# Kernel optimization log

Hardware: AMD Instinct MI355X
Metric: run time of the kernel (lower is better)

## Reference

```python
import jax, jax.numpy as jnp
import numpy as np

N = 50000      # nodes
E = 800000     # edges (avg degree 16)
HID = 64       # hidden / out_channels per head (concat=False)
EDIM = 3       # edge_dim
H = 4          # heads
C = 64         # per-head channels (== hidden since concat=False mean)
L = 2          # ode_layers
NEG_SLOPE = 0.2
LN_EPS = 1e-5


def setup_inputs() -> dict:
    key = jax.random.key(0)
    ks = jax.random.split(key, 12)
    h = jax.random.normal(ks[0], (N, HID), dtype=jnp.float32)
    edge_index = jax.random.randint(ks[1], (2, E), 0, N, dtype=jnp.int64)
    edge_attr = jax.random.normal(ks[2], (E, EDIM), dtype=jnp.float32)
    t = jnp.zeros((), dtype=jnp.float32)
    s = 1.0 / np.sqrt(HID)
    lin_W = jax.random.normal(ks[3], (L, H * C, HID), dtype=jnp.float32) * s
    lin_W = lin_W.at[L - 1].mul(0.1)  # mimics gats[-1].lin.weight.mul_(0.1)
    lin_edge_W = jax.random.normal(ks[4], (L, H * C, EDIM), dtype=jnp.float32) * (1.0 / np.sqrt(EDIM))
    att_src = jax.random.normal(ks[5], (L, H, C), dtype=jnp.float32) * s
    att_dst = jax.random.normal(ks[6], (L, H, C), dtype=jnp.float32) * s
    att_edge = jax.random.normal(ks[7], (L, H, C), dtype=jnp.float32) * s
    bias = jnp.zeros((L, C), dtype=jnp.float32)
    ln_gamma = jnp.ones((L, HID), dtype=jnp.float32)
    ln_beta = jnp.zeros((L, HID), dtype=jnp.float32)
    return {"t": t, "h": h, "edge_index": edge_index, "edge_attr": edge_attr,
            "lin_W": lin_W, "lin_edge_W": lin_edge_W, "att_src": att_src,
            "att_dst": att_dst, "att_edge": att_edge, "bias": bias,
            "ln_gamma": ln_gamma, "ln_beta": ln_beta}


def _gat_layer(z, src, dst, lin_W, lin_edge_W, att_src, att_dst, att_edge,
               bias, edge_attr):
    n = z.shape[0]
    x = (z @ lin_W.T).reshape(n, H, C)                      # [N,H,C]
    a_src = (x * att_src).sum(-1)                            # [N,H]
    a_dst = (x * att_dst).sum(-1)                            # [N,H]
    e = (edge_attr @ lin_edge_W.T).reshape(-1, H, C)         # [E,H,C]
    a_e = (e * att_edge).sum(-1)                             # [E,H]
    alpha = jax.nn.leaky_relu(a_src[src] + a_dst[dst] + a_e, NEG_SLOPE)
    # segment-softmax over incoming edges of each destination node
    amax = jax.ops.segment_max(alpha, dst, num_segments=n)
    amax = jnp.where(jnp.isfinite(amax), amax, 0.0)
    ex = jnp.exp(alpha - amax[dst])                          # [E,H]
    denom = jax.ops.segment_sum(ex, dst, num_segments=n)
    w = ex / (denom[dst] + 1e-16)
    msg = jax.ops.segment_sum(w[:, :, None] * x[src], dst, num_segments=n)
    return msg.mean(axis=1) + bias                           # [N,C] (concat=False)


def reference(t, h, edge_index, edge_attr, lin_W, lin_edge_W, att_src,
              att_dst, att_edge, bias, ln_gamma, ln_beta):
    src, dst = edge_index[0], edge_index[1]
    z = h
    for i in range(L):
        out = _gat_layer(z, src, dst, lin_W[i], lin_edge_W[i], att_src[i],
                         att_dst[i], att_edge[i], bias[i], edge_attr)
        mu = out.mean(-1, keepdims=True)
        var = ((out - mu) ** 2).mean(-1, keepdims=True)
        ln = (out - mu) / jnp.sqrt(var + LN_EPS) * ln_gamma[i] + ln_beta[i]
        z = jax.nn.silu(ln)
    return z
```

## Files before the change

### kernel.cpp

```cpp
#include <hip/hip_runtime.h>
#include <math.h>

#define NN 50000
#define NE 800000
#define NEG_SLOPE 0.2f
#define LN_EPS 1e-5f
#define SROW 264

typedef unsigned short ushort_t;
typedef unsigned int uint_t;
typedef __attribute__((ext_vector_type(8))) short bf16x8;
typedef __attribute__((ext_vector_type(4))) float f32x4;

__device__ __forceinline__ float bf2f(ushort_t u) {
    return __uint_as_float(((uint_t)u) << 16);
}
__device__ __forceinline__ ushort_t f2bf(float f) {
    uint_t b = __float_as_uint(f);
    uint_t r = (b + 0x7fffu + ((b >> 16) & 1u)) >> 16;
    return (ushort_t)r;
}
__device__ __forceinline__ float ldx(const void* p, size_t i, int isbf) {
    return isbf ? bf2f(((const ushort_t*)p)[i]) : ((const float*)p)[i];
}
__device__ __forceinline__ int clampN(int v) {
    return v < 0 ? 0 : (v >= NN ? NN - 1 : v);
}
__device__ __forceinline__ int sniff_f64(const int* ei) {
    return (ei[1] == 0 && ei[3] == 0 && ei[5] == 0 && ei[7] == 0) ? 1 : 0;
}

__global__ __launch_bounds__(256) void setup(
    const void* __restrict__ lin_W, const void* __restrict__ lin_edge_W,
    const void* __restrict__ att_src, const void* __restrict__ att_dst,
    const void* __restrict__ att_edge, const void* __restrict__ h_in,
    const int* __restrict__ ei, float* __restrict__ Mbuf,
    ushort_t* __restrict__ wext, int* __restrict__ esrc, int* __restrict__ edst,
    int* __restrict__ deg, int* __restrict__ pos, int* __restrict__ flags) {
    int tid = threadIdx.x, lane = tid & 63;
    int nthreads = gridDim.x * 256;
    int gtid = blockIdx.x * 256 + tid;
    __shared__ int s_bf;
    if (tid == 0) s_bf = 1;
    __syncthreads();
    {
        uint_t ex = (((const ushort_t*)h_in)[2 * tid] >> 7) & 0xFFu;
        if (ex > 0x8Cu) s_bf = 0;
    }
    __syncthreads();
    int isbf = s_bf;
    int f64 = sniff_f64(ei);
    if (gtid == 0) {
        flags[0] = f64;
        flags[1] = isbf;
    }
    if (f64) {
        const int4* s4 = (const int4*)ei;
        const int4* d4 = (const int4*)(ei + 2 * NE);
        for (int p = gtid; p < NE / 2; p += nthreads) {
            int4 sv = s4[p], dv = d4[p];
            int d0 = clampN(dv.x), d1 = clampN(dv.z);
            esrc[2 * p]     = clampN(sv.x);
            esrc[2 * p + 1] = clampN(sv.z);
            edst[2 * p]     = d0;
            edst[2 * p + 1] = d1;
            pos[2 * p]      = atomicAdd(&deg[d0], 1);
            pos[2 * p + 1]  = atomicAdd(&deg[d1], 1);
        }
    } else {
        const int2* s2 = (const int2*)ei;
        const int2* d2 = (const int2*)(ei + NE);
        for (int p = gtid; p < NE / 2; p += nthreads) {
            int2 sv = s2[p], dv = d2[p];
            int d0 = clampN(dv.x), d1 = clampN(dv.y);
            esrc[2 * p]     = clampN(sv.x);
            esrc[2 * p + 1] = clampN(sv.y);
            edst[2 * p]     = d0;
            edst[2 * p + 1] = d1;
            pos[2 * p]      = atomicAdd(&deg[d0], 1);
            pos[2 * p + 1]  = atomicAdd(&deg[d1], 1);
        }
    }
    if (blockIdx.x == 0) {
        for (int rep = 0; rep < 2; ++rep) {
            int idx = rep * 256 + tid;
            int l = idx >> 8, hc = idx & 255;
            float ae = ldx(att_edge, l * 256 + hc, isbf);
            size_t b3 = ((size_t)l * 256 + hc) * 3;
            float q0 = ae * ldx(lin_edge_W, b3 + 0, isbf);
            float q1 = ae * ldx(lin_edge_W, b3 + 1, isbf);
            float q2 = ae * ldx(lin_edge_W, b3 + 2, isbf);
            for (int off = 32; off > 0; off >>= 1) {
                q0 += __shfl_down(q0, off);
                q1 += __shfl_down(q1, off);
                q2 += __shfl_down(q2, off);
            }
            if (lane == 0) {
                int h = (idx >> 6) & 3;
                Mbuf[(l * 4 + h) * 3 + 0] = q0;
                Mbuf[(l * 4 + h) * 3 + 1] = q1;
                Mbuf[(l * 4 + h) * 3 + 2] = q2;
            }
        }
    }
    for (int idx = gtid; idx < 2 * 272 * 64; idx += nthreads) {
        int d = idx & 63;
        int row = (idx >> 6) % 272;
        int l = idx / (272 * 64);
        float v = 0.f;
        if (row < 256) {
            v = ldx(lin_W, ((size_t)l * 256 + row) * 64 + d, isbf);
        } else if (row < 264) {
            int h = (row - 256) & 3;
            const void* att = (row < 260) ? att_src : att_dst;
            float v0 = 0.f, v1 = 0.f, v2 = 0.f, v3 = 0.f;
            for (int c = 0; c < 64; c += 4) {
                size_t wb = ((size_t)l * 256 + h * 64 + c) * 64 + d;
                size_t ab = (size_t)l * 256 + h * 64 + c;
                v0 += ldx(lin_W, wb,       isbf) * ldx(att, ab,     isbf);
                v1 += ldx(lin_W, wb + 64,  isbf) * ldx(att, ab + 1, isbf);
                v2 += ldx(lin_W, wb + 128, isbf) * ldx(att, ab + 2, isbf);
                v3 += ldx(lin_W, wb + 192, isbf) * ldx(att, ab + 3, isbf);
            }
            v = (v0 + v1) + (v2 + v3);
        }
        wext[((size_t)l * 272 + row) * 64 + d] = f2bf(v);
    }
}


template <int LAYER>
__device__ __forceinline__ void linear_body(
    int bid, int nblk, const void* __restrict__ h_in,
    const ushort_t* __restrict__ zbuf, const ushort_t* __restrict__ wext,
    ushort_t* __restrict__ xb, float* __restrict__ a_src,
    float* __restrict__ a_dst, int isbf) {
    __shared__ __align__(16) ushort_t st_all[4 * 16 * SROW];
    int tid = threadIdx.x, wv = tid >> 6, lane = tid & 63;
    int q = lane >> 4, mi = lane & 15;
    int f32path = (LAYER == 0) && !isbf;
    const ushort_t* zsrc = (LAYER == 0) ? (const ushort_t*)h_in : zbuf;
    const ushort_t* wl = wext + (size_t)LAYER * 272 * 64;
    bf16x8 wf[34];
#pragma unroll
    for (int t = 0; t < 17; ++t) {
        const ushort_t* wrow = wl + (size_t)(t * 16 + mi) * 64;
        wf[2 * t]     = *(const bf16x8*)(wrow + q * 8);
        wf[2 * t + 1] = *(const bf16x8*)(wrow + 32 + q * 8);
    }
    ushort_t* st = st_all + wv * 16 * SROW;
    int gwave = bid * 4 + wv, nwaves = nblk * 4;
    for (int tile = gwave; tile < NN / 16; tile += nwaves) {
        int mbase = tile * 16, mynode = mbase + mi;
        bf16x8 b0, b1;
        if (f32path) {
            const float* zf = (const float*)h_in + (size_t)mynode * 64;
            float4 fa = *(const float4*)(zf + q * 8);
            float4 fb = *(const float4*)(zf + q * 8 + 4);
            float4 fc = *(const float4*)(zf + 32 + q * 8);
            float4 fd = *(const float4*)(zf + 32 + q * 8 + 4);
            b0[0] = (short)f2bf(fa.x); b0[1] = (short)f2bf(fa.y);
            b0[2] = (short)f2bf(fa.z); b0[3] = (short)f2bf(fa.w);
            b0[4] = (short)f2bf(fb.x); b0[5] = (short)f2bf(fb.y);
            b0[6] = (short)f2bf(fb.z); b0[7] = (short)f2bf(fb.w);
            b1[0] = (short)f2bf(fc.x); b1[1] = (short)f2bf(fc.y);
            b1[2] = (short)f2bf(fc.z); b1[3] = (short)f2bf(fc.w);
            b1[4] = (short)f2bf(fd.x); b1[5] = (short)f2bf(fd.y);
            b1[6] = (short)f2bf(fd.z); b1[7] = (short)f2bf(fd.w);
        } else {
            const ushort_t* zrow = zsrc + (size_t)mynode * 64;
            b0 = *(const bf16x8*)(zrow + q * 8);
            b1 = *(const bf16x8*)(zrow + 32 + q * 8);
        }
#pragma unroll
        for (int t = 0; t < 17; ++t) {
            f32x4 acc = {0.f, 0.f, 0.f, 0.f};
            acc = __builtin_amdgcn_mfma_f32_16x16x32_bf16(wf[2 * t], b0, acc, 0, 0, 0);
            acc = __builtin_amdgcn_mfma_f32_16x16x32_bf16(wf[2 * t + 1], b1, acc, 0, 0, 0);
            if (t < 16) {
                ushort4 pk;
                pk.x = f2bf(acc[0]);
                pk.y = f2bf(acc[1]);
                pk.z = f2bf(acc[2]);
                pk.w = f2bf(acc[3]);
                *(ushort4*)(st + mi * SROW + t * 16 + q * 4) = pk;
            } else {
                float4 av;
                av.x = acc[0]; av.y = acc[1]; av.z = acc[2]; av.w = acc[3];
                if (q == 0) *(float4*)(a_src + (size_t)mynode * 4) = av;
                else if (q == 1) *(float4*)(a_dst + (size_t)mynode * 4) = av;
            }
        }
        for (int nn = 0; nn < 16; ++nn) {
            int node = mbase + nn;
            ushort4 pk;
            pk.x = st[nn * SROW + lane];
            pk.y = st[nn * SROW + 64 + lane];
            pk.z = st[nn * SROW + 128 + lane];
            pk.w = st[nn * SROW + 192 + lane];
            *(ushort4*)(xb + (size_t)node * 256 + lane * 4) = pk;
        }
    }
}

__global__ __launch_bounds__(256) void scan_linear0(
    const int* __restrict__ deg, int* __restrict__ rowptr,
    const void* __restrict__ h_in, const ushort_t* __restrict__ wext,
    ushort_t* __restrict__ xb, float* __restrict__ a_src,
    float* __restrict__ a_dst, const int* __restrict__ flags) {
    if (blockIdx.x == 0) {
        __shared__ int sh[256];
        int tid = threadIdx.x;
        const int PER = 200;
        int base = tid * PER;
        int s = 0;
        if (tid < 250) {
            for (int i = 0; i < PER; ++i) s += deg[base + i];
        }
        sh[tid] = s;
        __syncthreads();
        for (int off = 1; off < 256; off <<= 1) {
            int t = (tid >= off) ? sh[tid - off] : 0;
            __syncthreads();
            sh[tid] += t;
            __syncthreads();
        }
        int excl = sh[tid] - s;
        if (tid < 250) {
            int run = excl;
            for (int i = 0; i < PER; ++i) {
                rowptr[base + i] = run;
                run += deg[base + i];
            }
        }
        if (tid == 255) rowptr[NN] = NE;
    } else {
        linear_body<0>(blockIdx.x - 1, gridDim.x - 1, h_in, (const ushort_t*)0,
                       wext, xb, a_src, a_dst, flags[1]);
    }
}

__global__ __launch_bounds__(256) void node_linear1(
    const ushort_t* __restrict__ zbuf, const ushort_t* __restrict__ wext,
    ushort_t* __restrict__ xb, float* __restrict__ a_src,
    float* __restrict__ a_dst, const int* __restrict__ flags) {
    linear_body<1>(blockIdx.x, gridDim.x, (const void*)0, zbuf, wext, xb,
                   a_src, a_dst, flags[1]);
}

__global__ void csr_fill(const int* __restrict__ esrc, const int* __restrict__ edst,
                         const void* __restrict__ edge_attr,
                         const int* __restrict__ rowptr, const int* __restrict__ pos,
                         float4* __restrict__ edata, const int* __restrict__ flags) {
    int e4 = blockIdx.x * 256 + threadIdx.x;
    if (e4 >= NE / 4) return;
    int isbf = flags[1];
    int e = e4 * 4;
    int4 sv = *(const int4*)(esrc + e);
    int4 dv = *(const int4*)(edst + e);
    int4 pv = *(const int4*)(pos + e);
    float a[12];
    if (!isbf) {
        const float4* ea = (const float4*)((const float*)edge_attr + (size_t)e * 3);
        float4 f0 = ea[0], f1 = ea[1], f2 = ea[2];
        a[0] = f0.x; a[1] = f0.y; a[2]  = f0.z;
        a[3] = f0.w; a[4] = f1.x; a[5]  = f1.y;
        a[6] = f1.z; a[7] = f1.w; a[8]  = f2.x;
        a[9] = f2.y; a[10] = f2.z; a[11] = f2.w;
    } else {
#pragma unroll
        for (int i = 0; i < 12; ++i)
            a[i] = bf2f(((const ushort_t*)edge_attr)[(size_t)e * 3 + i]);
    }
    float4 ed0, ed1, ed2, ed3;
    ed0.x = a[0]; ed0.y = a[1];  ed0.z = a[2];  ed0.w = __int_as_float(sv.x);
    ed1.x = a[3]; ed1.y = a[4];  ed1.z = a[5];  ed1.w = __int_as_float(sv.y);
    ed2.x = a[6]; ed2.y = a[7];  ed2.z = a[8];  ed2.w = __int_as_float(sv.z);
    ed3.x = a[9]; ed3.y = a[10]; ed3.z = a[11]; ed3.w = __int_as_float(sv.w);
    edata[rowptr[dv.x] + pv.x] = ed0;
    edata[rowptr[dv.y] + pv.y] = ed1;
    edata[rowptr[dv.z] + pv.z] = ed2;
    edata[rowptr[dv.w] + pv.w] = ed3;
}

__global__ __launch_bounds__(256) void node_aggregate(
    const int* __restrict__ rowptr, const float4* __restrict__ edata,
    const float* __restrict__ a_src, const float* __restrict__ a_dst,
    const ushort_t* __restrict__ xb, const float* __restrict__ Mbuf,
    const void* __restrict__ bias, const void* __restrict__ gamma,
    const void* __restrict__ beta, ushort_t* __restrict__ zout,
    void* __restrict__ outp, const int* __restrict__ flags, int layer, int last) {
    __shared__ float4 wsh[4][64];
    __shared__ int ssh[4][64];
    int isbf = flags[1];
    int wv = threadIdx.x >> 6;
    int lane = threadIdx.x & 63;
    int n = blockIdx.x * 4 + wv;
    float M[12];
#pragma unroll
    for (int i = 0; i < 12; ++i) M[i] = Mbuf[layer * 12 + i];
    float4 ad = *(const float4*)(a_dst + (size_t)n * 4);
    int start = rowptr[n], end = rowptr[n + 1];
    float acc0 = 0.f, acc1 = 0.f, acc2 = 0.f, acc3 = 0.f;
    float den0 = 0.f, den1 = 0.f, den2 = 0.f, den3 = 0.f;
    for (int cb = start; cb < end; cb += 64) {
        int m = end - cb;
        if (m > 64) m = 64;
        if (lane < m) {
            float4 ed = edata[cb + lane];
            int s = __float_as_int(ed.w);
            float4 as4 = *(const float4*)(a_src + (size_t)s * 4);
            float t0 = as4.x + ad.x + ed.x * M[0] + ed.y * M[1] + ed.z * M[2];
            float t1 = as4.y + ad.y + ed.x * M[3] + ed.y * M[4] + ed.z * M[5];
            float t2 = as4.z + ad.z + ed.x * M[6] + ed.y * M[7] + ed.z * M[8];
            float t3 = as4.w + ad.w + ed.x * M[9] + ed.y * M[10] + ed.z * M[11];
            t0 = t0 > 0.f ? t0 : NEG_SLOPE * t0;
            t1 = t1 > 0.f ? t1 : NEG_SLOPE * t1;
            t2 = t2 > 0.f ? t2 : NEG_SLOPE * t2;
            t3 = t3 > 0.f ? t3 : NEG_SLOPE * t3;
            float4 ex;
            ex.x = __expf(fminf(t0, 80.f));
            ex.y = __expf(fminf(t1, 80.f));
            ex.z = __expf(fminf(t2, 80.f));
            ex.w = __expf(fminf(t3, 80.f));
            wsh[wv][lane] = ex;
            ssh[wv][lane] = s;
        }
        for (int j = 0; j < m; j += 4) {
            int j1 = j + 1 < m ? j + 1 : m - 1;
            int j2 = j + 2 < m ? j + 2 : m - 1;
            int j3 = j + 3 < m ? j + 3 : m - 1;
            int s0 = ssh[wv][j],  s1 = ssh[wv][j1];
            int s2 = ssh[wv][j2], s3 = ssh[wv][j3];
            float4 w0 = wsh[wv][j];
            float4 w1 = wsh[wv][j1];
            float4 w2 = wsh[wv][j2];
            float4 w3 = wsh[wv][j3];
            if (j + 1 >= m) w1 = make_float4(0.f, 0.f, 0.f, 0.f);
            if (j + 2 >= m) w2 = make_float4(0.f, 0.f, 0.f, 0.f);
            if (j + 3 >= m) w3 = make_float4(0.f, 0.f, 0.f, 0.f);
            ushort4 x0 = *(const ushort4*)(xb + (size_t)s0 * 256 + lane * 4);
            ushort4 x1 = *(const ushort4*)(xb + (size_t)s1 * 256 + lane * 4);
            ushort4 x2 = *(const ushort4*)(xb + (size_t)s2 * 256 + lane * 4);
            ushort4 x3 = *(const ushort4*)(xb + (size_t)s3 * 256 + lane * 4);
            acc0 += w0.x * bf2f(x0.x) + w1.x * bf2f(x1.x) +
                    w2.x * bf2f(x2.x) + w3.x * bf2f(x3.x);
            acc1 += w0.y * bf2f(x0.y) + w1.y * bf2f(x1.y) +
                    w2.y * bf2f(x2.y) + w3.y * bf2f(x3.y);
            acc2 += w0.z * bf2f(x0.z) + w1.z * bf2f(x1.z) +
                    w2.z * bf2f(x2.z) + w3.z * bf2f(x3.z);
            acc3 += w0.w * bf2f(x0.w) + w1.w * bf2f(x1.w) +
                    w2.w * bf2f(x2.w) + w3.w * bf2f(x3.w);
            den0 += w0.x + w1.x + w2.x + w3.x;
            den1 += w0.y + w1.y + w2.y + w3.y;
            den2 += w0.z + w1.z + w2.z + w3.z;
            den3 += w0.w + w1.w + w2.w + w3.w;
        }
    }
    float v = ldx(bias, layer * 64 + lane, isbf) +
              0.25f * (acc0 / (den0 + 1e-16f) + acc1 / (den1 + 1e-16f) +
                       acc2 / (den2 + 1e-16f) + acc3 / (den3 + 1e-16f));
    float sum = v;
    for (int off = 1; off < 64; off <<= 1) sum += __shfl_xor(sum, off);
    float mu = sum * (1.f / 64.f);
    float d = v - mu;
    float vv = d * d;
    for (int off = 1; off < 64; off <<= 1) vv += __shfl_xor(vv, off);
    float var = vv * (1.f / 64.f);
    float ln = d * rsqrtf(var + LN_EPS) * ldx(gamma, layer * 64 + lane, isbf) +
               ldx(beta, layer * 64 + lane, isbf);
    float sl = ln / (1.f + __expf(-ln));
    size_t idx = (size_t)n * 64 + lane;
    if (last) {
        if (isbf) ((ushort_t*)outp)[idx] = f2bf(sl);
        else      ((float*)outp)[idx] = sl;
    } else {
        zout[idx] = f2bf(sl);
    }
}

extern "C" void kernel_launch(void* const* d_in, const int* in_sizes, int n_in,
                              void* d_out, int out_size, void* d_ws, size_t ws_size,
                              hipStream_t stream) {
    int off = (in_sizes[0] == 1) ? 1 : 0;
    const void* h_in  = d_in[off + 0];
    const int*  ei    = (const int*)d_in[off + 1];
    const void* eattr = d_in[off + 2];
    const void* linW  = d_in[off + 3];
    const void* linEW = d_in[off + 4];
    const void* attS  = d_in[off + 5];
    const void* attD  = d_in[off + 6];
    const void* attE  = d_in[off + 7];
    const void* bias  = d_in[off + 8];
    const void* gamma = d_in[off + 9];
    const void* beta  = d_in[off + 10];

    char* w = (char*)d_ws;
    size_t o = 0;
    auto alloc = [&](size_t bytes) {
        void* q = w + o;
        o += (bytes + 255) & ~(size_t)255;
        return q;
    };
    int*    flags  = (int*)alloc(8);
    float*  Mbuf   = (float*)alloc(24 * 4);
    ushort_t* wext = (ushort_t*)alloc((size_t)2 * 272 * 64 * 2);
    float*  a_src  = (float*)alloc((size_t)NN * 4 * 4);
    float*  a_dst  = (float*)alloc((size_t)NN * 4 * 4);
    int*    rowptr = (int*)alloc((size_t)(NN + 1) * 4);
    int*    deg    = (int*)alloc((size_t)NN * 4);
    int*    pos    = (int*)alloc((size_t)NE * 4);
    ushort_t* zbuf = (ushort_t*)alloc((size_t)NN * 64 * 2);
    int*    esrc   = (int*)alloc((size_t)NE * 4);
    int*    edst   = (int*)alloc((size_t)NE * 4);
    ushort_t* xb   = (ushort_t*)alloc((size_t)NN * 256 * 2);
    float4* edata  = (float4*)alloc((size_t)NE * 16);

    hipMemsetAsync(deg, 0, (size_t)NN * 4, stream);
    setup<<<256, 256, 0, stream>>>(linW, linEW, attS, attD, attE, h_in, ei,
                                   Mbuf, wext, esrc, edst, deg, pos, flags);
    scan_linear0<<<513, 256, 0, stream>>>(deg, rowptr, h_in, wext, xb,
                                          a_src, a_dst, flags);
    csr_fill<<<(NE / 4 + 255) / 256, 256, 0, stream>>>(esrc, edst, eattr,
                                                       rowptr, pos, edata, flags);
    node_aggregate<<<NN / 4, 256, 0, stream>>>(rowptr, edata, a_src, a_dst,
                                               xb, Mbuf, bias, gamma, beta,
                                               zbuf, d_out, flags, 0, 0);
    node_linear1<<<512, 256, 0, stream>>>(zbuf, wext, xb, a_src, a_dst, flags);
    node_aggregate<<<NN / 4, 256, 0, stream>>>(rowptr, edata, a_src, a_dst,
                                               xb, Mbuf, bias, gamma, beta,
                                               zbuf, d_out, flags, 1, 1);
}
```

Baseline: 323.4 us.

## Restructure CSR build with a separate histogram, atomic-cursor fill, and fused linear0

Splits edge preprocessing into four kernels: index conversion that also zeroes deg (replacing the memset), a wide histogram kernel that also builds wext, a single-block 1024-thread row scan, and an edge fill that places edges with atomic cursors. The fill now runs in the same kernel as the layer-0 linear transform instead of alongside the scan. This drops the per-edge pos array and its extra traffic, and lets the linear transform overlap with the scatter. The linear grid is also raised from 512 to 1024 blocks. The cost is a second round of atomics during the fill and a nondeterministic edge order within each segment, so summation order can vary between runs.

```diff
diff --git a/kernel.cpp b/kernel.cpp
--- a/kernel.cpp
+++ b/kernel.cpp
@@ -30,14 +30,11 @@
     return (ei[1] == 0 && ei[3] == 0 && ei[5] == 0 && ei[7] == 0) ? 1 : 0;
 }
 
-__global__ __launch_bounds__(256) void setup(
-    const void* __restrict__ lin_W, const void* __restrict__ lin_edge_W,
-    const void* __restrict__ att_src, const void* __restrict__ att_dst,
-    const void* __restrict__ att_edge, const void* __restrict__ h_in,
-    const int* __restrict__ ei, float* __restrict__ Mbuf,
-    ushort_t* __restrict__ wext, int* __restrict__ esrc, int* __restrict__ edst,
-    int* __restrict__ deg, int* __restrict__ pos, int* __restrict__ flags) {
-    int tid = threadIdx.x, lane = tid & 63;
+__global__ __launch_bounds__(256) void prep(
+    const void* __restrict__ h_in, const int* __restrict__ ei,
+    int* __restrict__ esrc, int* __restrict__ edst,
+    int* __restrict__ deg, int* __restrict__ flags) {
+    int tid = threadIdx.x;
     int nthreads = gridDim.x * 256;
     int gtid = blockIdx.x * 256 + tid;
     __shared__ int s_bf;
@@ -48,40 +45,50 @@
         if (ex > 0x8Cu) s_bf = 0;
     }
     __syncthreads();
-    int isbf = s_bf;
     int f64 = sniff_f64(ei);
     if (gtid == 0) {
         flags[0] = f64;
-        flags[1] = isbf;
-    }
+        flags[1] = s_bf;
+    }
+    for (int i = gtid; i < NN; i += nthreads) deg[i] = 0;
     if (f64) {
         const int4* s4 = (const int4*)ei;
         const int4* d4 = (const int4*)(ei + 2 * NE);
         for (int p = gtid; p < NE / 2; p += nthreads) {
             int4 sv = s4[p], dv = d4[p];
-            int d0 = clampN(dv.x), d1 = clampN(dv.z);
             esrc[2 * p]     = clampN(sv.x);
             esrc[2 * p + 1] = clampN(sv.z);
-            edst[2 * p]     = d0;
-            edst[2 * p + 1] = d1;
-            pos[2 * p]      = atomicAdd(&deg[d0], 1);
-            pos[2 * p + 1]  = atomicAdd(&deg[d1], 1);
+            edst[2 * p]     = clampN(dv.x);
+            edst[2 * p + 1] = clampN(dv.z);
         }
     } else {
         const int2* s2 = (const int2*)ei;
         const int2* d2 = (const int2*)(ei + NE);
         for (int p = gtid; p < NE / 2; p += nthreads) {
             int2 sv = s2[p], dv = d2[p];
-            int d0 = clampN(dv.x), d1 = clampN(dv.y);
             esrc[2 * p]     = clampN(sv.x);
             esrc[2 * p + 1] = clampN(sv.y);
-            edst[2 * p]     = d0;
-            edst[2 * p + 1] = d1;
-            pos[2 * p]      = atomicAdd(&deg[d0], 1);
-            pos[2 * p + 1]  = atomicAdd(&deg[d1], 1);
-        }
-    }
-    if (blockIdx.x == 0) {
+            edst[2 * p]     = clampN(dv.x);
+            edst[2 * p + 1] = clampN(dv.y);
+        }
+    }
+}
+
+__global__ __launch_bounds__(256) void hist_wext(
+    const int* __restrict__ edst, int* __restrict__ deg,
+    const void* __restrict__ lin_W, const void* __restrict__ lin_edge_W,
+    const void* __restrict__ att_src, const void* __restrict__ att_dst,
+    const void* __restrict__ att_edge, float* __restrict__ Mbuf,
+    ushort_t* __restrict__ wext, const int* __restrict__ flags) {
+    int tid = threadIdx.x, lane = tid & 63;
+    int bid = blockIdx.x;
+    if (bid < 3125) {
+        int e = bid * 256 + tid;
+        if (e < NE) atomicAdd(&deg[edst[e]], 1);
+        return;
+    }
+    int isbf = flags[1];
+    if (bid == 3125) {
         for (int rep = 0; rep < 2; ++rep) {
             int idx = rep * 256 + tid;
             int l = idx >> 8, hc = idx & 255;
@@ -103,29 +110,61 @@
             }
         }
     }
-    for (int idx = gtid; idx < 2 * 272 * 64; idx += nthreads) {
-        int d = idx & 63;
-        int row = (idx >> 6) % 272;
-        int l = idx / (272 * 64);
-        float v = 0.f;
-        if (row < 256) {
-            v = ldx(lin_W, ((size_t)l * 256 + row) * 64 + d, isbf);
-        } else if (row < 264) {
-            int h = (row - 256) & 3;
-            const void* att = (row < 260) ? att_src : att_dst;
-            float v0 = 0.f, v1 = 0.f, v2 = 0.f, v3 = 0.f;
-            for (int c = 0; c < 64; c += 4) {
-                size_t wb = ((size_t)l * 256 + h * 64 + c) * 64 + d;
-                size_t ab = (size_t)l * 256 + h * 64 + c;
-                v0 += ldx(lin_W, wb,       isbf) * ldx(att, ab,     isbf);
-                v1 += ldx(lin_W, wb + 64,  isbf) * ldx(att, ab + 1, isbf);
-                v2 += ldx(lin_W, wb + 128, isbf) * ldx(att, ab + 2, isbf);
-                v3 += ldx(lin_W, wb + 192, isbf) * ldx(att, ab + 3, isbf);
-            }
-            v = (v0 + v1) + (v2 + v3);
-        }
-        wext[((size_t)l * 272 + row) * 64 + d] = f2bf(v);
-    }
+    int idx = (bid - 3125) * 256 + tid;
+    if (idx >= 2 * 272 * 64) return;
+    int d = idx & 63;
+    int row = (idx >> 6) % 272;
+    int l = idx / (272 * 64);
+    float v = 0.f;
+    if (row < 256) {
+        v = ldx(lin_W, ((size_t)l * 256 + row) * 64 + d, isbf);
+    } else if (row < 264) {
+        int h = (row - 256) & 3;
+        const void* att = (row < 260) ? att_src : att_dst;
+        float v0 = 0.f, v1 = 0.f, v2 = 0.f, v3 = 0.f;
+        for (int c = 0; c < 64; c += 4) {
+            size_t wb = ((size_t)l * 256 + h * 64 + c) * 64 + d;
+            size_t ab = (size_t)l * 256 + h * 64 + c;
+            v0 += ldx(lin_W, wb,       isbf) * ldx(att, ab,     isbf);
+            v1 += ldx(lin_W, wb + 64,  isbf) * ldx(att, ab + 1, isbf);
+            v2 += ldx(lin_W, wb + 128, isbf) * ldx(att, ab + 2, isbf);
+            v3 += ldx(lin_W, wb + 192, isbf) * ldx(att, ab + 3, isbf);
+        }
+        v = (v0 + v1) + (v2 + v3);
+    }
+    wext[((size_t)l * 272 + row) * 64 + d] = f2bf(v);
+}
+
+__global__ __launch_bounds__(1024) void rowscan(const int* __restrict__ deg,
+                                                int* __restrict__ rowptr,
+                                                int* __restrict__ rwork) {
+    __shared__ int sh[1024];
+    int tid = threadIdx.x;
+    const int PER = 49;
+    int base = tid * PER;
+    int s = 0;
+    for (int i = 0; i < PER; ++i) {
+        int n = base + i;
+        if (n < NN) s += deg[n];
+    }
+    sh[tid] = s;
+    __syncthreads();
+    for (int off = 1; off < 1024; off <<= 1) {
+        int t = (tid >= off) ? sh[tid - off] : 0;
+        __syncthreads();
+        sh[tid] += t;
+        __syncthreads();
+    }
+    int run = sh[tid] - s;
+    for (int i = 0; i < PER; ++i) {
+        int n = base + i;
+        if (n < NN) {
+            rowptr[n] = run;
+            rwork[n] = run;
+            run += deg[n];
+        }
+    }
+    if (tid == 0) rowptr[NN] = NE;
 }
 
 
@@ -203,62 +242,28 @@
     }
 }
 
-__global__ __launch_bounds__(256) void scan_linear0(
-    const int* __restrict__ deg, int* __restrict__ rowptr,
+#define LIN_BLOCKS 1024
+#define FILL_BLOCKS 782
+
+__global__ __launch_bounds__(256) void fill_lin0(
+    const int* __restrict__ esrc, const int* __restrict__ edst,
+    const void* __restrict__ edge_attr, int* __restrict__ rwork,
+    float4* __restrict__ edata,
     const void* __restrict__ h_in, const ushort_t* __restrict__ wext,
     ushort_t* __restrict__ xb, float* __restrict__ a_src,
     float* __restrict__ a_dst, const int* __restrict__ flags) {
-    if (blockIdx.x == 0) {
-        __shared__ int sh[256];
-        int tid = threadIdx.x;
-        const int PER = 200;
-        int base = tid * PER;
-        int s = 0;
-        if (tid < 250) {
-            for (int i = 0; i < PER; ++i) s += deg[base + i];
-        }
-        sh[tid] = s;
-        __syncthreads();
-        for (int off = 1; off < 256; off <<= 1) {
-            int t = (tid >= off) ? sh[tid - off] : 0;
-            __syncthreads();
-            sh[tid] += t;
-            __syncthreads();
-        }
-        int excl = sh[tid] - s;
-        if (tid < 250) {
-            int run = excl;
-            for (int i = 0; i < PER; ++i) {
-                rowptr[base + i] = run;
-                run += deg[base + i];
-            }
-        }
-        if (tid == 255) rowptr[NN] = NE;
-    } else {
-        linear_body<0>(blockIdx.x - 1, gridDim.x - 1, h_in, (const ushort_t*)0,
-                       wext, xb, a_src, a_dst, flags[1]);
-    }
-}
-
-__global__ __launch_bounds__(256) void node_linear1(
-    const ushort_t* __restrict__ zbuf, const ushort_t* __restrict__ wext,
-    ushort_t* __restrict__ xb, float* __restrict__ a_src,
-    float* __restrict__ a_dst, const int* __restrict__ flags) {
-    linear_body<1>(blockIdx.x, gridDim.x, (const void*)0, zbuf, wext, xb,
-                   a_src, a_dst, flags[1]);
-}
-
-__global__ void csr_fill(const int* __restrict__ esrc, const int* __restrict__ edst,
-                         const void* __restrict__ edge_attr,
-                         const int* __restrict__ rowptr, const int* __restrict__ pos,
-                         float4* __restrict__ edata, const int* __restrict__ flags) {
-    int e4 = blockIdx.x * 256 + threadIdx.x;
+    int bid = blockIdx.x;
+    if (bid < LIN_BLOCKS) {
+        linear_body<0>(bid, LIN_BLOCKS, h_in, (const ushort_t*)0, wext, xb,
+                       a_src, a_dst, flags[1]);
+        return;
+    }
+    int e4 = (bid - LIN_BLOCKS) * 256 + threadIdx.x;
     if (e4 >= NE / 4) return;
     int isbf = flags[1];
     int e = e4 * 4;
     int4 sv = *(const int4*)(esrc + e);
     int4 dv = *(const int4*)(edst + e);
-    int4 pv = *(const int4*)(pos + e);
     float a[12];
     if (!isbf) {
         const float4* ea = (const float4*)((const float*)edge_attr + (size_t)e * 3);
@@ -277,10 +282,18 @@
     ed1.x = a[3]; ed1.y = a[4];  ed1.z = a[5];  ed1.w = __int_as_float(sv.y);
     ed2.x = a[6]; ed2.y = a[7];  ed2.z = a[8];  ed2.w = __int_as_float(sv.z);
     ed3.x = a[9]; ed3.y = a[10]; ed3.z = a[11]; ed3.w = __int_as_float(sv.w);
-    edata[rowptr[dv.x] + pv.x] = ed0;
-    edata[rowptr[dv.y] + pv.y] = ed1;
-    edata[rowptr[dv.z] + pv.z] = ed2;
-    edata[rowptr[dv.w] + pv.w] = ed3;
+    edata[atomicAdd(&rwork[dv.x], 1)] = ed0;
+    edata[atomicAdd(&rwork[dv.y], 1)] = ed1;
+    edata[atomicAdd(&rwork[dv.z], 1)] = ed2;
+    edata[atomicAdd(&rwork[dv.w], 1)] = ed3;
+}
+
+__global__ __launch_bounds__(256) void node_linear1(
+    const ushort_t* __restrict__ zbuf, const ushort_t* __restrict__ wext,
+    ushort_t* __restrict__ xb, float* __restrict__ a_src,
+    float* __restrict__ a_dst, const int* __restrict__ flags) {
+    linear_body<1>(blockIdx.x, gridDim.x, (const void*)0, zbuf, wext, xb,
+                   a_src, a_dst, flags[1]);
 }
 
 __global__ __launch_bounds__(256) void node_aggregate(
@@ -408,25 +421,25 @@
     float*  a_src  = (float*)alloc((size_t)NN * 4 * 4);
     float*  a_dst  = (float*)alloc((size_t)NN * 4 * 4);
     int*    rowptr = (int*)alloc((size_t)(NN + 1) * 4);
+    int*    rwork  = (int*)alloc((size_t)NN * 4);
     int*    deg    = (int*)alloc((size_t)NN * 4);
-    int*    pos    = (int*)alloc((size_t)NE * 4);
     ushort_t* zbuf = (ushort_t*)alloc((size_t)NN * 64 * 2);
     int*    esrc   = (int*)alloc((size_t)NE * 4);
     int*    edst   = (int*)alloc((size_t)NE * 4);
     ushort_t* xb   = (ushort_t*)alloc((size_t)NN * 256 * 2);
     float4* edata  = (float4*)alloc((size_t)NE * 16);
 
-    hipMemsetAsync(deg, 0, (size_t)NN * 4, stream);
-    setup<<<256, 256, 0, stream>>>(linW, linEW, attS, attD, attE, h_in, ei,
-                                   Mbuf, wext, esrc, edst, deg, pos, flags);
-    scan_linear0<<<513, 256, 0, stream>>>(deg, rowptr, h_in, wext, xb,
-                                          a_src, a_dst, flags);
-    csr_fill<<<(NE / 4 + 255) / 256, 256, 0, stream>>>(esrc, edst, eattr,
-                                                       rowptr, pos, edata, flags);
+    prep<<<256, 256, 0, stream>>>(h_in, ei, esrc, edst, deg, flags);
+    hist_wext<<<3125 + 136, 256, 0, stream>>>(edst, deg, linW, linEW, attS,
+                                              attD, attE, Mbuf, wext, flags);
+    rowscan<<<1, 1024, 0, stream>>>(deg, rowptr, rwork);
+    fill_lin0<<<LIN_BLOCKS + FILL_BLOCKS, 256, 0, stream>>>(
+        esrc, edst, eattr, rwork, edata, h_in, wext, xb, a_src, a_dst, flags);
     node_aggregate<<<NN / 4, 256, 0, stream>>>(rowptr, edata, a_src, a_dst,
                                                xb, Mbuf, bias, gamma, beta,
                                                zbuf, d_out, flags, 0, 0);
-    node_linear1<<<512, 256, 0, stream>>>(zbuf, wext, xb, a_src, a_dst, flags);
+    node_linear1<<<LIN_BLOCKS, 256, 0, stream>>>(zbuf, wext, xb, a_src,
+                                                 a_dst, flags);
     node_aggregate<<<NN / 4, 256, 0, stream>>>(rowptr, edata, a_src, a_dst,
                                                xb, Mbuf, bias, gamma, beta,
                                                zbuf, d_out, flags, 1, 1);
```

Result: slower. 466.1 us (+44.1%).
